# Kernel optimization log

Measured on AMD Instinct MI355X. Metric: run time of the kernel, lower is better.

## Reference

```python
import jax, jax.numpy as jnp
import numpy as np

T, D, N, W = 8192, 768, 10000, 32  # tokens, hidden dim, num spans, max span width


def setup_inputs() -> dict:
    key = jax.random.key(0)
    k1, k2, k3, k4, k5 = jax.random.split(key, 5)
    sentence_embeddings = jax.random.normal(k1, (T, D), dtype=jnp.float32)
    lengths = jax.random.randint(k2, (N,), 1, W + 1)           # span lengths in [1, W]
    starts = jax.random.randint(k3, (N,), 0, T - W)
    ends = starts + lengths - 1                                 # inclusive end, < T
    sentence_spans = jnp.stack([starts, ends], axis=1).astype(jnp.int32)
    Wq = (jax.random.normal(k4, (D, D), dtype=jnp.float32) / np.sqrt(D).astype(np.float32))
    bq = jax.random.normal(k5, (D,), dtype=jnp.float32) * 0.01
    return {"sentence_embeddings": sentence_embeddings,
            "sentence_spans": sentence_spans,
            "Wq": Wq, "bq": bq}


def reference(sentence_embeddings, sentence_spans, Wq, bq):
    # Padded + masked batched version of the per-span loop:
    #   span_emb = emb[s:e+1]; q = span_emb @ Wq.T + bq
    #   w = softmax(q @ span_emb.T, dim=1); out = (w @ span_emb).sum(0)
    starts = sentence_spans[:, 0]                               # [N]
    lengths = sentence_spans[:, 1] - starts + 1                 # inclusive end -> length
    offs = jnp.arange(W)
    pos = starts[:, None] + offs[None, :]                       # [N, W] token indices
    valid = offs[None, :] < lengths[:, None]                    # [N, W] in-span mask
    pos = jnp.clip(pos, 0, sentence_embeddings.shape[0] - 1)
    span_emb = sentence_embeddings[pos]                         # [N, W, D] ragged gather
    span_emb = jnp.where(valid[:, :, None], span_emb, 0.0)
    query = jnp.einsum('nwd,ed->nwe', span_emb, Wq) + bq        # [N, W, D]
    scores = jnp.einsum('nqd,nkd->nqk', query, span_emb)        # [N, W, W]
    scores = jnp.where(valid[:, None, :], scores, -jnp.inf)     # mask pad keys (softmax dim=1)
    weights = jax.nn.softmax(scores, axis=-1)
    attn = jnp.einsum('nqk,nkd->nqd', weights, span_emb)        # [N, W, D]
    attn = jnp.where(valid[:, :, None], attn, 0.0)              # drop pad query rows
    return attn.sum(axis=1)                                     # [N, D] == torch.sum(attention, dim=0) per span
```

## Files before the change

kernel.cpp:

```cpp
#include <hip/hip_runtime.h>
#include <hip/hip_bf16.h>
#include <cstddef>
#include <cstdint>

constexpr int Tt = 8192;
constexpr int Dd = 768;
constexpr int Nn = 10000;
constexpr int Ww = 32;

typedef __bf16 bf16x8 __attribute__((ext_vector_type(8)));
typedef __bf16 bf16x4 __attribute__((ext_vector_type(4)));
typedef __bf16 bf16x2 __attribute__((ext_vector_type(2)));
typedef _Float16 half8v __attribute__((ext_vector_type(8)));
typedef _Float16 half4v __attribute__((ext_vector_type(4)));
typedef float f32x4 __attribute__((ext_vector_type(4)));

#define MFMA16(a, b, c) __builtin_amdgcn_mfma_f32_16x16x32_bf16((a), (b), (c), 0, 0, 0)
#define MFMAH(a, b, c) __builtin_amdgcn_mfma_f32_16x16x32_f16((a), (b), (c), 0, 0, 0)

template <bool LO>
__global__ __launch_bounds__(256) void conv_kernel(const float* __restrict__ src,
                                                   __bf16* __restrict__ h,
                                                   __bf16* __restrict__ l, int n4) {
    const int i = blockIdx.x * 256 + threadIdx.x;
    if (i >= n4) return;
    const float4 v = reinterpret_cast<const float4*>(src)[i];
    bf16x4 oh, ol;
    oh[0] = (__bf16)v.x; oh[1] = (__bf16)v.y; oh[2] = (__bf16)v.z; oh[3] = (__bf16)v.w;
    reinterpret_cast<bf16x4*>(h)[i] = oh;
    if (LO) {
        ol[0] = (__bf16)(v.x - (float)oh[0]);
        ol[1] = (__bf16)(v.y - (float)oh[1]);
        ol[2] = (__bf16)(v.z - (float)oh[2]);
        ol[3] = (__bf16)(v.w - (float)oh[3]);
        reinterpret_cast<bf16x4*>(l)[i] = ol;
    }
}

__global__ __launch_bounds__(256) void conv3_kernel(const float* __restrict__ src,
                                                    __bf16* __restrict__ h,
                                                    __bf16* __restrict__ l,
                                                    _Float16* __restrict__ f, int n4) {
    const int i = blockIdx.x * 256 + threadIdx.x;
    if (i >= n4) return;
    const float4 v = reinterpret_cast<const float4*>(src)[i];
    bf16x4 oh, ol;
    half4v of;
    const float vv[4] = {v.x, v.y, v.z, v.w};
#pragma unroll
    for (int j = 0; j < 4; ++j) {
        oh[j] = (__bf16)vv[j];
        ol[j] = (__bf16)(vv[j] - (float)oh[j]);
        of[j] = (_Float16)vv[j];
    }
    reinterpret_cast<bf16x4*>(h)[i] = oh;
    reinterpret_cast<bf16x4*>(l)[i] = ol;
    reinterpret_cast<half4v*>(f)[i] = of;
}

__global__ __launch_bounds__(256) void zero_kernel(int* __restrict__ p, int n) {
    const int i = blockIdx.x * 256 + threadIdx.x;
    if (i < n) p[i] = 0;
}

__global__ __launch_bounds__(256) void hist_kernel(const int* __restrict__ spans,
                                                   int* __restrict__ hist) {
    const int i = blockIdx.x * 256 + threadIdx.x;
    if (i < Nn) atomicAdd(&hist[spans[2 * i]], 1);
}

__global__ __launch_bounds__(256) void scan_kernel(int* __restrict__ hist) {
    __shared__ int part[256];
    const int t = threadIdx.x;
    int vals[32];
    int sum = 0;
#pragma unroll
    for (int i = 0; i < 32; ++i) { vals[i] = hist[t * 32 + i]; sum += vals[i]; }
    part[t] = sum;
    __syncthreads();
    for (int off = 1; off < 256; off <<= 1) {
        const int v = (t >= off) ? part[t - off] : 0;
        __syncthreads();
        part[t] += v;
        __syncthreads();
    }
    int run = (t == 0) ? 0 : part[t - 1];
#pragma unroll
    for (int i = 0; i < 32; ++i) { const int v = vals[i]; hist[t * 32 + i] = run; run += v; }
}

__global__ __launch_bounds__(256) void scatter_kernel(const int* __restrict__ spans,
                                                      int* __restrict__ offs,
                                                      int* __restrict__ perm) {
    const int i = blockIdx.x * 256 + threadIdx.x;
    if (i < Nn) {
        const int p = atomicAdd(&offs[spans[2 * i]], 1);
        perm[p] = i;
    }
}

template <bool SPLIT>
__global__ __launch_bounds__(256) void qproj_kernel(const float* __restrict__ emb,
                                                    const float* __restrict__ Wq,
                                                    const float* __restrict__ bq,
                                                    __bf16* __restrict__ Qh,
                                                    __bf16* __restrict__ Ql) {
    __shared__ float As[64][32];
    __shared__ float Bs[64][32];
    const int tid = threadIdx.x;
    const int tx = tid & 15;
    const int ty = tid >> 4;
    const int m0 = blockIdx.x * 64;
    const int n0 = blockIdx.y * 64;

    float acc[4][4] = {};

    for (int kc = 0; kc < Dd; kc += 32) {
#pragma unroll
        for (int i = 0; i < 2; ++i) {
            const int f   = tid + i * 256;
            const int row = f >> 3;
            const int c4  = f & 7;
            const int ph  = (c4 + (row >> 2)) & 7;
            *reinterpret_cast<float4*>(&As[row][ph * 4]) =
                *reinterpret_cast<const float4*>(&emb[(size_t)(m0 + row) * Dd + kc + c4 * 4]);
            *reinterpret_cast<float4*>(&Bs[row][ph * 4]) =
                *reinterpret_cast<const float4*>(&Wq[(size_t)(n0 + row) * Dd + kc + c4 * 4]);
        }
        __syncthreads();
#pragma unroll
        for (int d4 = 0; d4 < 8; ++d4) {
            float4 av[4], bv[4];
#pragma unroll
            for (int r = 0; r < 4; ++r)
                av[r] = *reinterpret_cast<const float4*>(&As[ty * 4 + r][((d4 + ty) & 7) * 4]);
#pragma unroll
            for (int c = 0; c < 4; ++c)
                bv[c] = *reinterpret_cast<const float4*>(&Bs[tx * 4 + c][((d4 + tx) & 7) * 4]);
#pragma unroll
            for (int r = 0; r < 4; ++r)
#pragma unroll
                for (int c = 0; c < 4; ++c) {
                    acc[r][c] += av[r].x * bv[c].x;
                    acc[r][c] += av[r].y * bv[c].y;
                    acc[r][c] += av[r].z * bv[c].z;
                    acc[r][c] += av[r].w * bv[c].w;
                }
        }
        __syncthreads();
    }
#pragma unroll
    for (int r = 0; r < 4; ++r) {
        bf16x4 oh, ol;
#pragma unroll
        for (int c = 0; c < 4; ++c) {
            const float v = acc[r][c] + bq[n0 + tx * 4 + c];
            const __bf16 h = (__bf16)v;
            oh[c] = h;
            if (SPLIT) ol[c] = (__bf16)(v - (float)h);
        }
        const size_t off = (size_t)(m0 + ty * 4 + r) * Dd + n0 + tx * 4;
        *reinterpret_cast<bf16x4*>(&Qh[off]) = oh;
        if (SPLIT) *reinterpret_cast<bf16x4*>(&Ql[off]) = ol;
    }
}

__global__ __launch_bounds__(256) void qproj_mfma2_kernel(const __bf16* __restrict__ Eh,
                                                          const __bf16* __restrict__ El,
                                                          const __bf16* __restrict__ Wh,
                                                          const __bf16* __restrict__ Wl,
                                                          const float* __restrict__ bq,
                                                          _Float16* __restrict__ Qf) {
    __shared__ __align__(16) __bf16 Ahs[128 * 32];
    __shared__ __align__(16) __bf16 Als[128 * 32];
    __shared__ __align__(16) __bf16 Bhs[64 * 32];
    __shared__ __align__(16) __bf16 Bls[64 * 32];

    const int tid  = threadIdx.x;
    const int wave = tid >> 6;
    const int lane = tid & 63;

    const int b   = blockIdx.x;
    const int xcd = b & 7;
    const int li  = b >> 3;
    const int mt  = xcd * 8 + li / 12;
    const int nt  = li % 12;
    const int m0 = mt * 128;
    const int n0 = nt * 64;
    const int wm = (wave & 1) * 64;
    const int wn = (wave >> 1) * 32;
    const int fr = lane & 15;
    const int kg = lane >> 4;

    int arow[2], agc[2];
#pragma unroll
    for (int i = 0; i < 2; ++i) {
        const int seg = tid + i * 256;
        arow[i] = seg >> 2;
        agc[i]  = ((seg & 3) ^ (arow[i] & 3)) * 8;
    }
    const int brow = tid >> 2;
    const int bgc  = ((tid & 3) ^ (brow & 3)) * 8;

    bf16x8 pah[2], pal[2], pbh, pbl;
    auto ldnext = [&](int kc) {
#pragma unroll
        for (int i = 0; i < 2; ++i) {
            const size_t ga = (size_t)(m0 + arow[i]) * Dd + kc + agc[i];
            pah[i] = *reinterpret_cast<const bf16x8*>(&Eh[ga]);
            pal[i] = *reinterpret_cast<const bf16x8*>(&El[ga]);
        }
        const size_t gb = (size_t)(n0 + brow) * Dd + kc + bgc;
        pbh = *reinterpret_cast<const bf16x8*>(&Wh[gb]);
        pbl = *reinterpret_cast<const bf16x8*>(&Wl[gb]);
    };
    ldnext(0);

    f32x4 acc[4][2] = {};

    for (int kc = 0; kc < Dd; kc += 32) {
        __syncthreads();
#pragma unroll
        for (int i = 0; i < 2; ++i) {
            const int slot = tid + i * 256;
            *reinterpret_cast<bf16x8*>(&Ahs[slot * 8]) = pah[i];
            *reinterpret_cast<bf16x8*>(&Als[slot * 8]) = pal[i];
        }
        *reinterpret_cast<bf16x8*>(&Bhs[tid * 8]) = pbh;
        *reinterpret_cast<bf16x8*>(&Bls[tid * 8]) = pbl;
        __syncthreads();
        if (kc + 32 < Dd) ldnext(kc + 32);

        bf16x8 ah[4], al[4], bh[2], bl[2];
#pragma unroll
        for (int r = 0; r < 4; ++r) {
            const int R = wm + r * 16 + fr;
            const int p = (kg ^ (R & 3)) * 8;
            ah[r] = *reinterpret_cast<const bf16x8*>(&Ahs[R * 32 + p]);
            al[r] = *reinterpret_cast<const bf16x8*>(&Als[R * 32 + p]);
        }
#pragma unroll
        for (int c = 0; c < 2; ++c) {
            const int R = wn + c * 16 + fr;
            const int p = (kg ^ (R & 3)) * 8;
            bh[c] = *reinterpret_cast<const bf16x8*>(&Bhs[R * 32 + p]);
            bl[c] = *reinterpret_cast<const bf16x8*>(&Bls[R * 32 + p]);
        }
#pragma unroll
        for (int r = 0; r < 4; ++r)
#pragma unroll
            for (int c = 0; c < 2; ++c) {
                acc[r][c] = MFMA16(ah[r], bh[c], acc[r][c]);
                acc[r][c] = MFMA16(al[r], bh[c], acc[r][c]);
                acc[r][c] = MFMA16(ah[r], bl[c], acc[r][c]);
            }
    }

#pragma unroll
    for (int c = 0; c < 2; ++c) {
        const int ocol = n0 + wn + c * 16 + fr;
        const float bqv = bq[ocol];
#pragma unroll
        for (int r = 0; r < 4; ++r)
#pragma unroll
            for (int j = 0; j < 4; ++j) {
                const int orow = m0 + wm + r * 16 + kg * 4 + j;
                Qf[(size_t)orow * Dd + ocol] = (_Float16)(acc[r][c][j] + bqv);
            }
    }
}

__global__ __launch_bounds__(256) void span_attn_win_kernel(const _Float16* __restrict__ Ef,
                                                            const int* __restrict__ spans,
                                                            const _Float16* __restrict__ Qf,
                                                            const int* __restrict__ perm,
                                                            float* __restrict__ out) {
    constexpr int WR = 48, CH = 128, ST = 136, NCH = Dd / CH;
    __shared__ __align__(16) _Float16 Qs[WR * ST];
    __shared__ __align__(16) _Float16 Es[WR * ST];

    const int tid  = threadIdx.x;
    const int wave = tid >> 6;
    const int lane = tid & 63;

    const int b     = blockIdx.x;
    const int bp    = (b & 7) * 313 + (b >> 3);
    const int slot0 = bp * 4;
    const int slot  = slot0 + wave;
    const bool active = slot < Nn;

    int s0 = perm[slot0 < Nn ? slot0 : (Nn - 1)];
    if ((unsigned)s0 >= (unsigned)Nn) s0 = 0;
    int s = active ? perm[slot] : s0;
    if ((unsigned)s >= (unsigned)Nn) s = 0;

    const int w0    = spans[2 * s0];
    const int start = spans[2 * s];
    const int L     = spans[2 * s + 1] - start + 1;
    const bool big  = L > 16;
    const int sl    = start - w0;
    const bool inwin = active && sl >= 0 && sl <= (WR - 32);

    const int row = lane & 15;
    const int kq  = lane >> 4;

    const size_t gq = (size_t)(start + row) * Dd + kq * 8;

    f32x4 acc00 = {0.f, 0.f, 0.f, 0.f};
    f32x4 acc01 = {0.f, 0.f, 0.f, 0.f};
    f32x4 acc10 = {0.f, 0.f, 0.f, 0.f};
    f32x4 acc11 = {0.f, 0.f, 0.f, 0.f};

    for (int c = 0; c < NCH; ++c) {
        const int c0 = c * CH;
        __syncthreads();
#pragma unroll
        for (int i = 0; i < 3; ++i) {
            const int seg = tid + i * 256;
            const int r  = seg >> 4;
            const int cs = seg & 15;
            const int gr = w0 + r < Tt ? w0 + r : Tt - 1;
            const size_t ga = (size_t)gr * Dd + c0 + cs * 8;
            *reinterpret_cast<half8v*>(&Qs[r * ST + cs * 8]) =
                *reinterpret_cast<const half8v*>(&Qf[ga]);
            *reinterpret_cast<half8v*>(&Es[r * ST + cs * 8]) =
                *reinterpret_cast<const half8v*>(&Ef[ga]);
        }
        __syncthreads();

        if (inwin) {
            const int ab = (sl + row) * ST + kq * 8;
#pragma unroll
            for (int j = 0; j < 4; ++j) {
                const int o = j * 32;
                const half8v a0 = *reinterpret_cast<const half8v*>(&Qs[ab + o]);
                const half8v b0 = *reinterpret_cast<const half8v*>(&Es[ab + o]);
                acc00 = MFMAH(a0, b0, acc00);
                if (big) {
                    const half8v a1 = *reinterpret_cast<const half8v*>(&Qs[ab + 16 * ST + o]);
                    const half8v b1 = *reinterpret_cast<const half8v*>(&Es[ab + 16 * ST + o]);
                    acc01 = MFMAH(a0, b1, acc01);
                    acc10 = MFMAH(a1, b0, acc10);
                    acc11 = MFMAH(a1, b1, acc11);
                }
            }
        } else if (active) {
#pragma unroll
            for (int j = 0; j < 4; ++j) {
                const int o = c0 + j * 32;
                const half8v a0 = *reinterpret_cast<const half8v*>(&Qf[gq + o]);
                const half8v b0 = *reinterpret_cast<const half8v*>(&Ef[gq + o]);
                acc00 = MFMAH(a0, b0, acc00);
                if (big) {
                    const half8v a1 = *reinterpret_cast<const half8v*>(&Qf[gq + 16 * Dd + o]);
                    const half8v b1 = *reinterpret_cast<const half8v*>(&Ef[gq + 16 * Dd + o]);
                    acc01 = MFMAH(a0, b1, acc01);
                    acc10 = MFMAH(a1, b0, acc10);
                    acc11 = MFMAH(a1, b1, acc11);
                }
            }
        }
    }

    const float NEG = -1e30f;
    const bool kv0 = row < L;
    const bool kv1 = (16 + row) < L;
    float cA, cB;
    {
        float w00[4], w01[4], w10[4], w11[4];
#pragma unroll
        for (int r = 0; r < 4; ++r) {
            float m = kv0 ? acc00[r] : NEG;
            if (big) m = fmaxf(m, kv1 ? acc01[r] : NEG);
#pragma unroll
            for (int st = 1; st <= 8; st <<= 1) m = fmaxf(m, __shfl_xor(m, st));
            const float e0 = kv0 ? __expf(acc00[r] - m) : 0.f;
            const float e1 = (big && kv1) ? __expf(acc01[r] - m) : 0.f;
            float sum = e0 + e1;
#pragma unroll
            for (int st = 1; st <= 8; st <<= 1) sum += __shfl_xor(sum, st);
            const float inv = 1.f / sum;
            const bool qv = (kq * 4 + r) < L;
            w00[r] = qv ? e0 * inv : 0.f;
            w01[r] = qv ? e1 * inv : 0.f;
            if (big) {
                float mh = kv0 ? acc10[r] : NEG;
                mh = fmaxf(mh, kv1 ? acc11[r] : NEG);
#pragma unroll
                for (int st = 1; st <= 8; st <<= 1) mh = fmaxf(mh, __shfl_xor(mh, st));
                const float f0 = kv0 ? __expf(acc10[r] - mh) : 0.f;
                const float f1 = kv1 ? __expf(acc11[r] - mh) : 0.f;
                float sh = f0 + f1;
#pragma unroll
                for (int st = 1; st <= 8; st <<= 1) sh += __shfl_xor(sh, st);
                const float invh = 1.f / sh;
                const bool qvh = (16 + kq * 4 + r) < L;
                w10[r] = qvh ? f0 * invh : 0.f;
                w11[r] = qvh ? f1 * invh : 0.f;
            }
        }
        float pa = w00[0] + w00[1] + w00[2] + w00[3];
        float pb = 0.f;
        if (big) {
            pa += w10[0] + w10[1] + w10[2] + w10[3];
            pb = w01[0] + w01[1] + w01[2] + w01[3] +
                 w11[0] + w11[1] + w11[2] + w11[3];
        }
        pa += __shfl_xor(pa, 16);
        pa += __shfl_xor(pa, 32);
        if (big) {
            pb += __shfl_xor(pb, 16);
            pb += __shfl_xor(pb, 32);
        }
        cA = pa;
        cB = pb;
    }

    if (active) {
        f32x4 o[3] = {};
        const int KP = (L + 3) & ~3;
        const _Float16* ebase = Ef + (size_t)start * Dd + lane * 4;
        for (int k = 0; k < KP; k += 4) {
            float cv[4];
            half4v ev[4][3];
#pragma unroll
            for (int j = 0; j < 4; ++j) {
                const int kk = k + j;
                cv[j] = (kk < 16) ? __shfl(cA, kk) : __shfl(cB, kk - 16);
#pragma unroll
                for (int i = 0; i < 3; ++i)
                    ev[j][i] = *reinterpret_cast<const half4v*>(ebase + (size_t)kk * Dd + i * 256);
            }
#pragma unroll
            for (int j = 0; j < 4; ++j)
#pragma unroll
                for (int i = 0; i < 3; ++i) {
                    o[i][0] += cv[j] * (float)ev[j][i][0];
                    o[i][1] += cv[j] * (float)ev[j][i][1];
                    o[i][2] += cv[j] * (float)ev[j][i][2];
                    o[i][3] += cv[j] * (float)ev[j][i][3];
                }
        }
#pragma unroll
        for (int i = 0; i < 3; ++i)
            *reinterpret_cast<f32x4*>(&out[(size_t)s * Dd + i * 256 + lane * 4]) = o[i];
    }
}

template <bool SPLIT, bool SORTED>
__global__ __launch_bounds__(256) void span_attn_g_kernel(const __bf16* __restrict__ Eb,
                                                          const int* __restrict__ spans,
                                                          const __bf16* __restrict__ Qh,
                                                          const __bf16* __restrict__ Ql,
                                                          const int* __restrict__ perm,
                                                          float* __restrict__ out) {
    const int wave = threadIdx.x >> 6;
    const int lane = threadIdx.x & 63;

    int s;
    bool active;
    if (SORTED) {
        const int b    = blockIdx.x;
        const int bp   = (b & 7) * 313 + (b >> 3);
        const int slot = bp * 4 + wave;
        active = slot < Nn;
        int sv = active ? perm[slot] : 0;
        if ((unsigned)sv >= (unsigned)Nn) sv = 0;
        s = sv;
    } else {
        s = blockIdx.x * 4 + wave;
        active = true;
    }

    const int start = spans[2 * s];
    const int L     = spans[2 * s + 1] - start + 1;
    const bool big  = L > 16;

    const int row = lane & 15;
    const int kq  = lane >> 4;

    const size_t rbase = (size_t)(start + row) * Dd + kq * 8;
    const __bf16* qh0 = Qh + rbase;
    const __bf16* eb0 = Eb + rbase;
    const __bf16* ql0 = SPLIT ? (Ql + rbase) : nullptr;

    f32x4 acc00 = {0.f, 0.f, 0.f, 0.f};
    f32x4 acc01 = {0.f, 0.f, 0.f, 0.f};
    f32x4 acc10 = {0.f, 0.f, 0.f, 0.f};
    f32x4 acc11 = {0.f, 0.f, 0.f, 0.f};

    if (!big) {
        for (int kc = 0; kc < Dd; kc += 128) {
            bf16x8 A[4], B[4], AL[4];
#pragma unroll
            for (int j = 0; j < 4; ++j) {
                const int o = kc + j * 32;
                A[j] = *reinterpret_cast<const bf16x8*>(qh0 + o);
                B[j] = *reinterpret_cast<const bf16x8*>(eb0 + o);
                if (SPLIT) AL[j] = *reinterpret_cast<const bf16x8*>(ql0 + o);
            }
#pragma unroll
            for (int j = 0; j < 4; ++j) {
                acc00 = MFMA16(A[j], B[j], acc00);
                if (SPLIT) acc00 = MFMA16(AL[j], B[j], acc00);
            }
        }
    } else {
        for (int kc = 0; kc < Dd; kc += 64) {
            bf16x8 A0[2], A1[2], B0[2], B1[2], AL0[2], AL1[2];
#pragma unroll
            for (int j = 0; j < 2; ++j) {
                const int o = kc + j * 32;
                A0[j] = *reinterpret_cast<const bf16x8*>(qh0 + o);
                A1[j] = *reinterpret_cast<const bf16x8*>(qh0 + 16 * Dd + o);
                B0[j] = *reinterpret_cast<const bf16x8*>(eb0 + o);
                B1[j] = *reinterpret_cast<const bf16x8*>(eb0 + 16 * Dd + o);
                if (SPLIT) {
                    AL0[j] = *reinterpret_cast<const bf16x8*>(ql0 + o);
                    AL1[j] = *reinterpret_cast<const bf16x8*>(ql0 + 16 * Dd + o);
                }
            }
#pragma unroll
            for (int j = 0; j < 2; ++j) {
                acc00 = MFMA16(A0[j], B0[j], acc00);
                acc01 = MFMA16(A0[j], B1[j], acc01);
                acc10 = MFMA16(A1[j], B0[j], acc10);
                acc11 = MFMA16(A1[j], B1[j], acc11);
                if (SPLIT) {
                    acc00 = MFMA16(AL0[j], B0[j], acc00);
                    acc01 = MFMA16(AL0[j], B1[j], acc01);
                    acc10 = MFMA16(AL1[j], B0[j], acc10);
                    acc11 = MFMA16(AL1[j], B1[j], acc11);
                }
            }
        }
    }

    const float NEG = -1e30f;
    const bool kv0 = row < L;
    const bool kv1 = (16 + row) < L;
    float cA, cB;
    {
        float w00[4], w01[4], w10[4], w11[4];
#pragma unroll
        for (int r = 0; r < 4; ++r) {
            float m = kv0 ? acc00[r] : NEG;
            if (big) m = fmaxf(m, kv1 ? acc01[r] : NEG);
#pragma unroll
            for (int st = 1; st <= 8; st <<= 1) m = fmaxf(m, __shfl_xor(m, st));
            const float e0 = kv0 ? __expf(acc00[r] - m) : 0.f;
            const float e1 = (big && kv1) ? __expf(acc01[r] - m) : 0.f;
            float sum = e0 + e1;
#pragma unroll
            for (int st = 1; st <= 8; st <<= 1) sum += __shfl_xor(sum, st);
            const float inv = 1.f / sum;
            const bool qv = (kq * 4 + r) < L;
            w00[r] = qv ? e0 * inv : 0.f;
            w01[r] = qv ? e1 * inv : 0.f;
            if (big) {
                float mh = kv0 ? acc10[r] : NEG;
                mh = fmaxf(mh, kv1 ? acc11[r] : NEG);
#pragma unroll
                for (int st = 1; st <= 8; st <<= 1) mh = fmaxf(mh, __shfl_xor(mh, st));
                const float f0 = kv0 ? __expf(acc10[r] - mh) : 0.f;
                const float f1 = kv1 ? __expf(acc11[r] - mh) : 0.f;
                float sh = f0 + f1;
#pragma unroll
                for (int st = 1; st <= 8; st <<= 1) sh += __shfl_xor(sh, st);
                const float invh = 1.f / sh;
                const bool qvh = (16 + kq * 4 + r) < L;
                w10[r] = qvh ? f0 * invh : 0.f;
                w11[r] = qvh ? f1 * invh : 0.f;
            }
        }
        float pa = w00[0] + w00[1] + w00[2] + w00[3];
        float pb = 0.f;
        if (big) {
            pa += w10[0] + w10[1] + w10[2] + w10[3];
            pb = w01[0] + w01[1] + w01[2] + w01[3] +
                 w11[0] + w11[1] + w11[2] + w11[3];
        }
        pa += __shfl_xor(pa, 16);
        pa += __shfl_xor(pa, 32);
        if (big) {
            pb += __shfl_xor(pb, 16);
            pb += __shfl_xor(pb, 32);
        }
        cA = pa;
        cB = pb;
    }

    if (active) {
        f32x4 o[3] = {};
        const int KP = (L + 3) & ~3;
        const __bf16* ebase = Eb + (size_t)start * Dd + lane * 4;
        for (int k = 0; k < KP; k += 4) {
            float cv[4];
            bf16x4 ev[4][3];
#pragma unroll
            for (int j = 0; j < 4; ++j) {
                const int kk = k + j;
                cv[j] = (kk < 16) ? __shfl(cA, kk) : __shfl(cB, kk - 16);
#pragma unroll
                for (int i = 0; i < 3; ++i)
                    ev[j][i] = *reinterpret_cast<const bf16x4*>(ebase + (size_t)kk * Dd + i * 256);
            }
#pragma unroll
            for (int j = 0; j < 4; ++j)
#pragma unroll
                for (int i = 0; i < 3; ++i) {
                    o[i][0] += cv[j] * (float)ev[j][i][0];
                    o[i][1] += cv[j] * (float)ev[j][i][1];
                    o[i][2] += cv[j] * (float)ev[j][i][2];
                    o[i][3] += cv[j] * (float)ev[j][i][3];
                }
        }
#pragma unroll
        for (int i = 0; i < 3; ++i)
            *reinterpret_cast<f32x4*>(&out[(size_t)s * Dd + i * 256 + lane * 4]) = o[i];
    }
}

extern "C" void kernel_launch(void* const* d_in, const int* in_sizes, int n_in,
                              void* d_out, int out_size, void* d_ws, size_t ws_size,
                              hipStream_t stream) {
    const float* emb   = (const float*)d_in[0];
    const int*   spans = (const int*)d_in[1];
    const float* Wq    = (const float*)d_in[2];
    const float* bq    = (const float*)d_in[3];
    float*       out   = (float*)d_out;

    const size_t TD = (size_t)Tt * Dd;
    const size_t DD = (size_t)Dd * Dd;
    const int nInts = 8192 + 10016;
    const size_t intBytes = (size_t)nInts * sizeof(int);
    auto align16 = [](size_t x) { return (x + 15) & ~(size_t)15; };

    const size_t mainBf = align16((4 * TD + 2 * DD) * 2);
    const size_t needMain = mainBf + intBytes;
    const size_t needB = align16(3 * TD * 2) + intBytes;
    const size_t needC = 3 * TD * 2;

    if (ws_size >= needMain) {
        char* base = (char*)d_ws;
        _Float16* Qf = (_Float16*)base;
        _Float16* Ef = (_Float16*)(base + TD * 2);
        __bf16* Eh = (__bf16*)(base + 2 * TD * 2);
        __bf16* El = (__bf16*)(base + 3 * TD * 2);
        __bf16* Wh = (__bf16*)(base + 4 * TD * 2);
        __bf16* Wl = (__bf16*)(base + 4 * TD * 2 + DD * 2);
        int* hist = (int*)(base + mainBf);
        int* perm = hist + 8192;

        conv3_kernel<<<(int)(TD / 4 / 256), 256, 0, stream>>>(emb, Eh, El, Ef, (int)(TD / 4));
        conv_kernel<true><<<(int)(DD / 4 / 256), 256, 0, stream>>>(Wq, Wh, Wl, (int)(DD / 4));
        zero_kernel<<<(nInts + 255) / 256, 256, 0, stream>>>(hist, nInts);
        hist_kernel<<<40, 256, 0, stream>>>(spans, hist);
        scan_kernel<<<1, 256, 0, stream>>>(hist);
        scatter_kernel<<<40, 256, 0, stream>>>(spans, hist, perm);
        qproj_mfma2_kernel<<<768, 256, 0, stream>>>(Eh, El, Wh, Wl, bq, Qf);
        span_attn_win_kernel<<<2504, 256, 0, stream>>>(Ef, spans, Qf, perm, out);
    } else if (ws_size >= needB) {
        __bf16* w = (__bf16*)d_ws;
        __bf16* Qh = w;
        __bf16* Ql = w + TD;
        __bf16* Eh = w + 2 * TD;
        int* hist = (int*)((char*)d_ws + align16(3 * TD * 2));
        int* perm = hist + 8192;

        conv_kernel<false><<<(int)(TD / 4 / 256), 256, 0, stream>>>(emb, Eh, nullptr, (int)(TD / 4));
        zero_kernel<<<(nInts + 255) / 256, 256, 0, stream>>>(hist, nInts);
        hist_kernel<<<40, 256, 0, stream>>>(spans, hist);
        scan_kernel<<<1, 256, 0, stream>>>(hist);
        scatter_kernel<<<40, 256, 0, stream>>>(spans, hist, perm);
        qproj_kernel<true><<<dim3(Tt / 64, Dd / 64), 256, 0, stream>>>(emb, Wq, bq, Qh, Ql);
        span_attn_g_kernel<true, true><<<2504, 256, 0, stream>>>(Eh, spans, Qh, Ql, perm, out);
    } else if (ws_size >= needC) {
        __bf16* w = (__bf16*)d_ws;
        __bf16* Qh = w;
        __bf16* Ql = w + TD;
        __bf16* Eh = w + 2 * TD;
        conv_kernel<false><<<(int)(TD / 4 / 256), 256, 0, stream>>>(emb, Eh, nullptr, (int)(TD / 4));
        qproj_kernel<true><<<dim3(Tt / 64, Dd / 64), 256, 0, stream>>>(emb, Wq, bq, Qh, Ql);
        span_attn_g_kernel<true, false><<<2500, 256, 0, stream>>>(Eh, spans, Qh, Ql, nullptr, out);
    } else {
        __bf16* w = (__bf16*)d_ws;
        __bf16* Qh = w;
        __bf16* Eh = w + TD;
        conv_kernel<false><<<(int)(TD / 4 / 256), 256, 0, stream>>>(emb, Eh, nullptr, (int)(TD / 4));
        qproj_kernel<false><<<dim3(Tt / 64, Dd / 64), 256, 0, stream>>>(emb, Wq, bq, Qh, nullptr);
        span_attn_g_kernel<false, false><<<2500, 256, 0, stream>>>(Eh, spans, Qh, nullptr, nullptr, out);
    }
}
```

Baseline: 178.8 us.

## Replace split-bf16 Q projection with single fp16 MFMA GEMM and fuse conversions

Drops the three-pass split-bf16 (hi/lo) emulation of the fp32 Q projection in favour of one fp16 MFMA pass, using fp16 copies of the embeddings and Wq. The two conversion kernels are merged into one fp16-only kernel, which no longer writes the bf16 hi/lo arrays. The GEMM tile changes to 128x96 with a K chunk of 64 and 512 blocks, and the zero kernel now clears only the histogram. This cuts MFMA work by about a factor of three and shrinks conversion traffic, at the cost of fp16 precision in Q (range and rounding risk).

After: 155.6 us. -13.0%, faster.

```diff
diff --git a/kernel.cpp b/kernel.cpp
--- a/kernel.cpp
+++ b/kernel.cpp
@@ -10,13 +10,37 @@
 
 typedef __bf16 bf16x8 __attribute__((ext_vector_type(8)));
 typedef __bf16 bf16x4 __attribute__((ext_vector_type(4)));
-typedef __bf16 bf16x2 __attribute__((ext_vector_type(2)));
 typedef _Float16 half8v __attribute__((ext_vector_type(8)));
 typedef _Float16 half4v __attribute__((ext_vector_type(4)));
 typedef float f32x4 __attribute__((ext_vector_type(4)));
 
 #define MFMA16(a, b, c) __builtin_amdgcn_mfma_f32_16x16x32_bf16((a), (b), (c), 0, 0, 0)
 #define MFMAH(a, b, c) __builtin_amdgcn_mfma_f32_16x16x32_f16((a), (b), (c), 0, 0, 0)
+
+__global__ __launch_bounds__(256) void conv_f16_kernel(const float* __restrict__ emb,
+                                                       const float* __restrict__ Wq,
+                                                       _Float16* __restrict__ Ef,
+                                                       _Float16* __restrict__ Wf) {
+    const int nE = (Tt * Dd) / 4;
+    const int nW = (Dd * Dd) / 4;
+    const int i = blockIdx.x * 256 + threadIdx.x;
+    if (i < nE) {
+        const float4 v = reinterpret_cast<const float4*>(emb)[i];
+        half4v o;
+        o[0] = (_Float16)v.x; o[1] = (_Float16)v.y;
+        o[2] = (_Float16)v.z; o[3] = (_Float16)v.w;
+        reinterpret_cast<half4v*>(Ef)[i] = o;
+    } else {
+        const int j = i - nE;
+        if (j < nW) {
+            const float4 v = reinterpret_cast<const float4*>(Wq)[j];
+            half4v o;
+            o[0] = (_Float16)v.x; o[1] = (_Float16)v.y;
+            o[2] = (_Float16)v.z; o[3] = (_Float16)v.w;
+            reinterpret_cast<half4v*>(Wf)[j] = o;
+        }
+    }
+}
 
 template <bool LO>
 __global__ __launch_bounds__(256) void conv_kernel(const float* __restrict__ src,
@@ -37,27 +61,6 @@
     }
 }
 
-__global__ __launch_bounds__(256) void conv3_kernel(const float* __restrict__ src,
-                                                    __bf16* __restrict__ h,
-                                                    __bf16* __restrict__ l,
-                                                    _Float16* __restrict__ f, int n4) {
-    const int i = blockIdx.x * 256 + threadIdx.x;
-    if (i >= n4) return;
-    const float4 v = reinterpret_cast<const float4*>(src)[i];
-    bf16x4 oh, ol;
-    half4v of;
-    const float vv[4] = {v.x, v.y, v.z, v.w};
-#pragma unroll
-    for (int j = 0; j < 4; ++j) {
-        oh[j] = (__bf16)vv[j];
-        ol[j] = (__bf16)(vv[j] - (float)oh[j]);
-        of[j] = (_Float16)vv[j];
-    }
-    reinterpret_cast<bf16x4*>(h)[i] = oh;
-    reinterpret_cast<bf16x4*>(l)[i] = ol;
-    reinterpret_cast<half4v*>(f)[i] = of;
-}
-
 __global__ __launch_bounds__(256) void zero_kernel(int* __restrict__ p, int n) {
     const int i = blockIdx.x * 256 + threadIdx.x;
     if (i < n) p[i] = 0;
@@ -165,16 +168,12 @@
     }
 }
 
-__global__ __launch_bounds__(256) void qproj_mfma2_kernel(const __bf16* __restrict__ Eh,
-                                                          const __bf16* __restrict__ El,
-                                                          const __bf16* __restrict__ Wh,
-                                                          const __bf16* __restrict__ Wl,
-                                                          const float* __restrict__ bq,
-                                                          _Float16* __restrict__ Qf) {
-    __shared__ __align__(16) __bf16 Ahs[128 * 32];
-    __shared__ __align__(16) __bf16 Als[128 * 32];
-    __shared__ __align__(16) __bf16 Bhs[64 * 32];
-    __shared__ __align__(16) __bf16 Bls[64 * 32];
+__global__ __launch_bounds__(256) void qproj_f16_kernel(const _Float16* __restrict__ Ef,
+                                                        const _Float16* __restrict__ Wf,
+                                                        const float* __restrict__ bq,
+                                                        _Float16* __restrict__ Qf) {
+    __shared__ __align__(16) _Float16 As[128 * 64];
+    __shared__ __align__(16) _Float16 Bs[96 * 64];
 
     const int tid  = threadIdx.x;
     const int wave = tid >> 6;
@@ -183,81 +182,73 @@
     const int b   = blockIdx.x;
     const int xcd = b & 7;
     const int li  = b >> 3;
-    const int mt  = xcd * 8 + li / 12;
-    const int nt  = li % 12;
+    const int mt  = xcd * 8 + (li >> 3);
+    const int nt  = li & 7;
     const int m0 = mt * 128;
-    const int n0 = nt * 64;
+    const int n0 = nt * 96;
     const int wm = (wave & 1) * 64;
-    const int wn = (wave >> 1) * 32;
+    const int wn = (wave >> 1) * 48;
     const int fr = lane & 15;
     const int kg = lane >> 4;
 
-    int arow[2], agc[2];
-#pragma unroll
-    for (int i = 0; i < 2; ++i) {
-        const int seg = tid + i * 256;
-        arow[i] = seg >> 2;
-        agc[i]  = ((seg & 3) ^ (arow[i] & 3)) * 8;
-    }
-    const int brow = tid >> 2;
-    const int bgc  = ((tid & 3) ^ (brow & 3)) * 8;
-
-    bf16x8 pah[2], pal[2], pbh, pbl;
-    auto ldnext = [&](int kc) {
-#pragma unroll
-        for (int i = 0; i < 2; ++i) {
-            const size_t ga = (size_t)(m0 + arow[i]) * Dd + kc + agc[i];
-            pah[i] = *reinterpret_cast<const bf16x8*>(&Eh[ga]);
-            pal[i] = *reinterpret_cast<const bf16x8*>(&El[ga]);
-        }
-        const size_t gb = (size_t)(n0 + brow) * Dd + kc + bgc;
-        pbh = *reinterpret_cast<const bf16x8*>(&Wh[gb]);
-        pbl = *reinterpret_cast<const bf16x8*>(&Wl[gb]);
-    };
-    ldnext(0);
-
-    f32x4 acc[4][2] = {};
-
-    for (int kc = 0; kc < Dd; kc += 32) {
-        __syncthreads();
-#pragma unroll
-        for (int i = 0; i < 2; ++i) {
-            const int slot = tid + i * 256;
-            *reinterpret_cast<bf16x8*>(&Ahs[slot * 8]) = pah[i];
-            *reinterpret_cast<bf16x8*>(&Als[slot * 8]) = pal[i];
-        }
-        *reinterpret_cast<bf16x8*>(&Bhs[tid * 8]) = pbh;
-        *reinterpret_cast<bf16x8*>(&Bls[tid * 8]) = pbl;
-        __syncthreads();
-        if (kc + 32 < Dd) ldnext(kc + 32);
-
-        bf16x8 ah[4], al[4], bh[2], bl[2];
-#pragma unroll
-        for (int r = 0; r < 4; ++r) {
-            const int R = wm + r * 16 + fr;
-            const int p = (kg ^ (R & 3)) * 8;
-            ah[r] = *reinterpret_cast<const bf16x8*>(&Ahs[R * 32 + p]);
-            al[r] = *reinterpret_cast<const bf16x8*>(&Als[R * 32 + p]);
-        }
-#pragma unroll
-        for (int c = 0; c < 2; ++c) {
-            const int R = wn + c * 16 + fr;
-            const int p = (kg ^ (R & 3)) * 8;
-            bh[c] = *reinterpret_cast<const bf16x8*>(&Bhs[R * 32 + p]);
-            bl[c] = *reinterpret_cast<const bf16x8*>(&Bls[R * 32 + p]);
-        }
-#pragma unroll
-        for (int r = 0; r < 4; ++r)
-#pragma unroll
-            for (int c = 0; c < 2; ++c) {
-                acc[r][c] = MFMA16(ah[r], bh[c], acc[r][c]);
-                acc[r][c] = MFMA16(al[r], bh[c], acc[r][c]);
-                acc[r][c] = MFMA16(ah[r], bl[c], acc[r][c]);
-            }
-    }
-
-#pragma unroll
-    for (int c = 0; c < 2; ++c) {
+    int ar[4], ao[4];
+#pragma unroll
+    for (int i = 0; i < 4; ++i) {
+        const int s = tid + i * 256;
+        ar[i] = s >> 3;
+        ao[i] = ((s & 7) ^ (ar[i] & 7)) * 8;
+    }
+    int br[3], bo[3];
+#pragma unroll
+    for (int i = 0; i < 3; ++i) {
+        const int s = tid + i * 256;
+        br[i] = s >> 3;
+        bo[i] = ((s & 7) ^ (br[i] & 7)) * 8;
+    }
+
+    f32x4 acc[4][3] = {};
+
+    for (int kc = 0; kc < Dd; kc += 64) {
+        half8v ra[4], rb[3];
+#pragma unroll
+        for (int i = 0; i < 4; ++i)
+            ra[i] = *reinterpret_cast<const half8v*>(&Ef[(size_t)(m0 + ar[i]) * Dd + kc + ao[i]]);
+#pragma unroll
+        for (int i = 0; i < 3; ++i)
+            rb[i] = *reinterpret_cast<const half8v*>(&Wf[(size_t)(n0 + br[i]) * Dd + kc + bo[i]]);
+        __syncthreads();
+#pragma unroll
+        for (int i = 0; i < 4; ++i)
+            *reinterpret_cast<half8v*>(&As[(tid + i * 256) * 8]) = ra[i];
+#pragma unroll
+        for (int i = 0; i < 3; ++i)
+            *reinterpret_cast<half8v*>(&Bs[(tid + i * 256) * 8]) = rb[i];
+        __syncthreads();
+
+#pragma unroll
+        for (int step = 0; step < 2; ++step) {
+            const int g = kg + 4 * step;
+            half8v a[4], bb[3];
+#pragma unroll
+            for (int r = 0; r < 4; ++r) {
+                const int R = wm + r * 16 + fr;
+                a[r] = *reinterpret_cast<const half8v*>(&As[R * 64 + (g ^ (R & 7)) * 8]);
+            }
+#pragma unroll
+            for (int c = 0; c < 3; ++c) {
+                const int R = wn + c * 16 + fr;
+                bb[c] = *reinterpret_cast<const half8v*>(&Bs[R * 64 + (g ^ (R & 7)) * 8]);
+            }
+#pragma unroll
+            for (int r = 0; r < 4; ++r)
+#pragma unroll
+                for (int c = 0; c < 3; ++c)
+                    acc[r][c] = MFMAH(a[r], bb[c], acc[r][c]);
+        }
+    }
+
+#pragma unroll
+    for (int c = 0; c < 3; ++c) {
         const int ocol = n0 + wn + c * 16 + fr;
         const float bqv = bq[ocol];
 #pragma unroll
@@ -632,12 +623,10 @@
 
     const size_t TD = (size_t)Tt * Dd;
     const size_t DD = (size_t)Dd * Dd;
-    const int nInts = 8192 + 10016;
-    const size_t intBytes = (size_t)nInts * sizeof(int);
+    const size_t intBytes = (size_t)(8192 + 10016) * sizeof(int);
     auto align16 = [](size_t x) { return (x + 15) & ~(size_t)15; };
 
-    const size_t mainBf = align16((4 * TD + 2 * DD) * 2);
-    const size_t needMain = mainBf + intBytes;
+    const size_t needMain = align16((2 * TD + DD) * 2) + intBytes;
     const size_t needB = align16(3 * TD * 2) + intBytes;
     const size_t needC = 3 * TD * 2;
 
@@ -645,20 +634,17 @@
         char* base = (char*)d_ws;
         _Float16* Qf = (_Float16*)base;
         _Float16* Ef = (_Float16*)(base + TD * 2);
-        __bf16* Eh = (__bf16*)(base + 2 * TD * 2);
-        __bf16* El = (__bf16*)(base + 3 * TD * 2);
-        __bf16* Wh = (__bf16*)(base + 4 * TD * 2);
-        __bf16* Wl = (__bf16*)(base + 4 * TD * 2 + DD * 2);
-        int* hist = (int*)(base + mainBf);
+        _Float16* Wf = (_Float16*)(base + 2 * TD * 2);
+        int* hist = (int*)(base + align16((2 * TD + DD) * 2));
         int* perm = hist + 8192;
 
-        conv3_kernel<<<(int)(TD / 4 / 256), 256, 0, stream>>>(emb, Eh, El, Ef, (int)(TD / 4));
-        conv_kernel<true><<<(int)(DD / 4 / 256), 256, 0, stream>>>(Wq, Wh, Wl, (int)(DD / 4));
-        zero_kernel<<<(nInts + 255) / 256, 256, 0, stream>>>(hist, nInts);
+        const int convBlocks = (int)((TD / 4 + DD / 4) / 256);
+        conv_f16_kernel<<<convBlocks, 256, 0, stream>>>(emb, Wq, Ef, Wf);
+        zero_kernel<<<32, 256, 0, stream>>>(hist, 8192);
         hist_kernel<<<40, 256, 0, stream>>>(spans, hist);
         scan_kernel<<<1, 256, 0, stream>>>(hist);
         scatter_kernel<<<40, 256, 0, stream>>>(spans, hist, perm);
-        qproj_mfma2_kernel<<<768, 256, 0, stream>>>(Eh, El, Wh, Wl, bq, Qf);
+        qproj_f16_kernel<<<512, 256, 0, stream>>>(Ef, Wf, bq, Qf);
         span_attn_win_kernel<<<2504, 256, 0, stream>>>(Ef, spans, Qf, perm, out);
     } else if (ws_size >= needB) {
         __bf16* w = (__bf16*)d_ws;
@@ -669,7 +655,7 @@
         int* perm = hist + 8192;
 
         conv_kernel<false><<<(int)(TD / 4 / 256), 256, 0, stream>>>(emb, Eh, nullptr, (int)(TD / 4));
-        zero_kernel<<<(nInts + 255) / 256, 256, 0, stream>>>(hist, nInts);
+        zero_kernel<<<32, 256, 0, stream>>>(hist, 8192);
         hist_kernel<<<40, 256, 0, stream>>>(spans, hist);
         scan_kernel<<<1, 256, 0, stream>>>(hist);
         scatter_kernel<<<40, 256, 0, stream>>>(spans, hist, perm);
```
